# Kernel tuning notes

Hardware: AMD Instinct MI355X
Metric: run time of the kernel (lower is better)

## Reference

```python
import jax, jax.numpy as jnp
import numpy as np

HEADS = 8
DIM_HEAD = 64
QUERY_DIM = 1024
CONTEXT_DIM = 768
INNER = HEADS * DIM_HEAD  # 512


def setup_inputs() -> dict:
    key = jax.random.key(0)
    ks = jax.random.split(key, 8)
    b, n, j = 4, 2048, 2048
    x = jax.random.normal(ks[0], (b, n, QUERY_DIM), dtype=jnp.float32)
    context = jax.random.normal(ks[1], (b, j, CONTEXT_DIM), dtype=jnp.float32)
    mask = jax.random.randint(ks[2], (b, j), 0, 2).astype(jnp.bool_)
    # weights stored as (in, out) so forward is x @ W (torch Linear stores transpose)
    W_q = jax.random.normal(ks[3], (QUERY_DIM, INNER), dtype=jnp.float32) / np.sqrt(QUERY_DIM)
    W_k = jax.random.normal(ks[4], (CONTEXT_DIM, INNER), dtype=jnp.float32) / np.sqrt(CONTEXT_DIM)
    W_v = jax.random.normal(ks[5], (CONTEXT_DIM, INNER), dtype=jnp.float32) / np.sqrt(CONTEXT_DIM)
    W_o = jax.random.normal(ks[6], (INNER, QUERY_DIM), dtype=jnp.float32) / np.sqrt(INNER)
    b_o = jax.random.normal(ks[7], (QUERY_DIM,), dtype=jnp.float32) * 0.01
    return {"x": x, "context": context, "mask": mask,
            "W_q": W_q, "W_k": W_k, "W_v": W_v, "W_o": W_o, "b_o": b_o}


def reference(x, context, mask, W_q, W_k, W_v, W_o, b_o):
    b, n, _ = x.shape
    j = context.shape[1]
    scale = DIM_HEAD ** -0.5
    # projections -> [b, n, h, d]
    q = (x @ W_q).reshape(b, n, HEADS, DIM_HEAD)
    k = (context @ W_k).reshape(b, j, HEADS, DIM_HEAD)
    v = (context @ W_v).reshape(b, j, HEADS, DIM_HEAD)
    # similarity [b, h, n, j]
    sim = jnp.einsum('bihd,bjhd->bhij', q, k) * scale
    max_neg = -jnp.finfo(sim.dtype).max
    sim = jnp.where(mask[:, None, None, :], sim, max_neg)
    attn = jax.nn.softmax(sim, axis=-1)
    out = jnp.einsum('bhij,bjhd->bihd', attn, v).reshape(b, n, INNER)
    return out @ W_o + b_o  # dropout is identity (p=0 / eval)
```

## Files before the change

### kernel.cpp

```cpp
#include <hip/hip_runtime.h>
#include <hip/hip_bf16.h>

typedef __attribute__((ext_vector_type(4)))  float  f32x4;
typedef __attribute__((ext_vector_type(16))) float  f32x16;
typedef __attribute__((ext_vector_type(8)))  short  bf16x8;
typedef __attribute__((ext_vector_type(4)))  int    int32x4;
typedef __attribute__((ext_vector_type(2)))  unsigned int uint32x2;

#define DEVINL static __device__ __forceinline__
#define GAS __attribute__((address_space(1)))
#define LAS __attribute__((address_space(3)))

DEVINL ushort f2bf(float f) {
  unsigned u = __builtin_bit_cast(unsigned, f);
  unsigned r = u + 0x7fffu + ((u >> 16) & 1u);
  return (ushort)(r >> 16);
}

DEVINL unsigned cvtpk(float lo, float hi) {
  unsigned r;
  asm("v_cvt_pk_bf16_f32 %0, %1, %2" : "=v"(r) : "v"(lo), "v"(hi));
  return r;
}

DEVINL void plswap(unsigned &a, unsigned &b) {
  asm("v_permlane32_swap_b32 %0, %1" : "+v"(a), "+v"(b));
}

DEVINL float bf2f(short s) {
  return __builtin_bit_cast(float, ((unsigned)(ushort)s) << 16);
}

DEVINL f32x4 mfma16(bf16x8 a, bf16x8 b, f32x4 c) {
  return __builtin_amdgcn_mfma_f32_16x16x32_bf16(a, b, c, 0, 0, 0);
}
DEVINL f32x16 mfma32(bf16x8 a, bf16x8 b, f32x16 c) {
  return __builtin_amdgcn_mfma_f32_32x32x16_bf16(a, b, c, 0, 0, 0);
}

__global__ __launch_bounds__(256)
void cvt_k(const float* __restrict__ x, const float* __restrict__ ctx,
           ushort* __restrict__ xb, ushort* __restrict__ cb,
           const int* __restrict__ msk, float* __restrict__ mb)
{
  const int NX = 8388608, NC = 6291456;
  int tid = blockIdx.x * 256 + threadIdx.x;
  if (tid < 8192) mb[tid] = msk[tid] ? 0.f : -1e30f;
  for (int i = tid; i < (NX + NC) / 8; i += 2048 * 256) {
    int e = i * 8;
    const float* s; ushort* d;
    if (e < NX) { s = x + e; d = xb + e; }
    else        { s = ctx + (e - NX); d = cb + (e - NX); }
    f32x4 v0 = *(const f32x4*)s;
    f32x4 v1 = *(const f32x4*)(s + 4);
    union { unsigned u[4]; int32x4 v; } pk;
    pk.u[0] = cvtpk(v0[0], v0[1]);
    pk.u[1] = cvtpk(v0[2], v0[3]);
    pk.u[2] = cvtpk(v1[0], v1[1]);
    pk.u[3] = cvtpk(v1[2], v1[3]);
    *(int32x4*)d = pk.v;
  }
}

__global__ __launch_bounds__(256)
void wtcvt_k(const float* __restrict__ Wq, const float* __restrict__ Wk,
             const float* __restrict__ Wv, const float* __restrict__ Wo,
             ushort* __restrict__ WqT, ushort* __restrict__ WkT,
             ushort* __restrict__ WvT, ushort* __restrict__ WoT)
{
  __shared__ ushort Ts[64][72];
  int id = blockIdx.x;
  const float* src; ushort* dst; int Kd, Nd, lid;
  if (id < 128)      { src = Wq; dst = WqT; Kd = 1024; Nd = 512;  lid = id; }
  else if (id < 224) { src = Wk; dst = WkT; Kd = 768;  Nd = 512;  lid = id - 128; }
  else if (id < 320) { src = Wv; dst = WvT; Kd = 768;  Nd = 512;  lid = id - 224; }
  else               { src = Wo; dst = WoT; Kd = 512;  Nd = 1024; lid = id - 320; }
  const int sh = (Nd == 512) ? 3 : 4;
  const int kb = lid >> sh, nb = lid & ((1 << sh) - 1);
  const int k0 = kb * 64, n0 = nb * 64;
  const int t = threadIdx.x;
  const int r = t >> 2, c0 = (t & 3) * 16;

  const float* sp = src + (size_t)(k0 + r) * Nd + n0 + c0;
  f32x4 v0 = *(const f32x4*)(sp);
  f32x4 v1 = *(const f32x4*)(sp + 4);
  f32x4 v2 = *(const f32x4*)(sp + 8);
  f32x4 v3 = *(const f32x4*)(sp + 12);
  #pragma unroll
  for (int e = 0; e < 4; e++) {
    Ts[c0 + e][r]      = f2bf(v0[e]);
    Ts[c0 + 4 + e][r]  = f2bf(v1[e]);
    Ts[c0 + 8 + e][r]  = f2bf(v2[e]);
    Ts[c0 + 12 + e][r] = f2bf(v3[e]);
  }
  __syncthreads();
  const int n = t >> 2, kc = (t & 3) * 16;
  bf16x8 o0 = *(const bf16x8*)&Ts[n][kc];
  bf16x8 o1 = *(const bf16x8*)&Ts[n][kc + 8];
  ushort* dp = dst + (size_t)(n0 + n) * Kd + k0 + kc;
  *(bf16x8*)dp       = o0;
  *(bf16x8*)(dp + 8) = o1;
}

template<int PHASE>
__global__ __launch_bounds__(256)
void mm_k(const ushort* __restrict__ xb, const ushort* __restrict__ cb,
          const ushort* __restrict__ WqT, const ushort* __restrict__ WkT,
          const ushort* __restrict__ WvT,
          ushort* __restrict__ Qb, ushort* __restrict__ Kb, ushort* __restrict__ VT,
          const ushort* __restrict__ AO, const ushort* __restrict__ WoT,
          float* __restrict__ out, const float* __restrict__ bias)
{
  __shared__ ushort As[2][128 * 32];
  __shared__ ushort Bs[2][128 * 32];

  const ushort* A; const ushort* BT; ushort* Cw = nullptr;
  int Kd, mode, m0, n0;
  if (PHASE == 0) {
    int id = blockIdx.x;
    id = (id & 7) * 96 + (id >> 3);
    const int which = id >> 8, local = id & 255;
    m0 = (local >> 2) * 128; n0 = (local & 3) * 128;
    if (which == 0)      { A = xb; BT = WqT; Cw = Qb; Kd = 1024; mode = 1; }
    else if (which == 1) { A = cb; BT = WkT; Cw = Kb; Kd = 768;  mode = 1; }
    else                 { A = cb; BT = WvT; Cw = VT; Kd = 768;  mode = 2; }
  } else {
    int id = blockIdx.x;
    id = (id & 7) * 64 + (id >> 3);
    m0 = (id >> 3) * 128; n0 = (id & 7) * 128;
    A = AO; BT = WoT; Kd = 512; mode = 0;
  }

  const int t = threadIdx.x, lane = t & 63, w = t >> 6;
  const int wr = w >> 1, wc = w & 1;
  const int g = lane >> 4, ql = lane & 15;

  const int srowo = 16 * w + (lane >> 2);
  const int sgg = (lane & 3) ^ ((lane >> 3) & 3);

  f32x4 acc[4][4];
  #pragma unroll
  for (int i = 0; i < 4; i++)
    #pragma unroll
    for (int j = 0; j < 4; j++) acc[i][j] = (f32x4){0.f, 0.f, 0.f, 0.f};

  auto stage = [&](int buf, int k0) {
    #pragma unroll
    for (int i = 0; i < 2; i++) {
      const int row = i * 64 + srowo;
      const ushort* asrc = A + (size_t)(m0 + row) * Kd + k0 + sgg * 8;
      __builtin_amdgcn_global_load_lds((const GAS void*)asrc,
          (LAS void*)&As[buf][(i * 64 + 16 * w) * 32], 16, 0, 0);
      const ushort* bsrc = BT + (size_t)(n0 + row) * Kd + k0 + sgg * 8;
      __builtin_amdgcn_global_load_lds((const GAS void*)bsrc,
          (LAS void*)&Bs[buf][(i * 64 + 16 * w) * 32], 16, 0, 0);
    }
  };

  const int NK = Kd >> 5;
  stage(0, 0);
  __syncthreads();

  const int sel = (ql >> 1) & 3;
  const int koff = (g ^ sel) * 8;

  for (int tt = 0; tt < NK; tt++) {
    const int cur = tt & 1;
    if (tt + 1 < NK) stage(cur ^ 1, (tt + 1) * 32);

    bf16x8 af[4], bfr[4];
    #pragma unroll
    for (int i = 0; i < 4; i++) {
      af[i]  = *(const bf16x8*)&As[cur][(wr * 64 + i * 16 + ql) * 32 + koff];
      bfr[i] = *(const bf16x8*)&Bs[cur][(wc * 64 + i * 16 + ql) * 32 + koff];
    }
    #pragma unroll
    for (int i = 0; i < 4; i++)
      #pragma unroll
      for (int j = 0; j < 4; j++)
        acc[i][j] = mfma16(af[i], bfr[j], acc[i][j]);
    __syncthreads();
  }

  #pragma unroll
  for (int i = 0; i < 4; i++) {
    #pragma unroll
    for (int j = 0; j < 4; j++) {
      int col = n0 + wc * 64 + j * 16 + ql;
      #pragma unroll
      for (int r = 0; r < 4; r++) {
        int mrow = m0 + wr * 64 + i * 16 + g * 4 + r;
        float v = acc[i][j][r];
        if (PHASE == 1) {
          out[(size_t)mrow * 1024 + col] = v + bias[col];
        } else {
          int b = mrow >> 11, nn = mrow & 2047;
          int hh = col >> 6, dd = col & 63;
          size_t base = (size_t)(b * 8 + hh) * 131072;
          if (mode == 1) Cw[base + (size_t)nn * 64 + dd]   = f2bf(v);
          else           Cw[base + (size_t)dd * 2048 + nn] = f2bf(v);
        }
      }
    }
  }
}

__global__ __launch_bounds__(256)
void attn_k(const ushort* __restrict__ Qb, const ushort* __restrict__ Kb,
            const ushort* __restrict__ VT, const float* __restrict__ mb,
            ushort* __restrict__ Opart, float2* __restrict__ Ml)
{
  constexpr int CHUNK = 512, NT = CHUNK / 64;
  __shared__ ushort Ks[2][64 * 64];
  __shared__ ushort Vs[2][64 * 64];

  const int bh = blockIdx.x, b = bh >> 3;
  const int sp = blockIdx.z;
  const int jb = sp * CHUNK;
  const int t = threadIdx.x, lane = t & 63, w = t >> 6;
  const int l31 = lane & 31, hi = lane >> 5;
  const int q0 = blockIdx.y * 128 + w * 32;

  const ushort* Qh = Qb + (size_t)bh * 131072;
  const ushort* Kh = Kb + (size_t)bh * 131072;
  const ushort* Vh = VT + (size_t)bh * 131072;
  const float* mp = mb + b * 2048 + 4 * hi;

  const int srow = lane >> 3;
  const int soff = ((lane & 7) * 16) ^ ((srow & 7) << 4);

  auto stage = [&](int buf, int j0) {
    const char* kg = (const char*)Kh + ((size_t)(j0 + 16 * w + srow)) * 128 + soff;
    __builtin_amdgcn_global_load_lds((const GAS void*)kg,
        (LAS void*)&Ks[buf][16 * w * 64], 16, 0, 0);
    __builtin_amdgcn_global_load_lds((const GAS void*)(kg + 1024),
        (LAS void*)&Ks[buf][(16 * w + 8) * 64], 16, 0, 0);
    const char* vg = (const char*)Vh + ((size_t)(16 * w + srow)) * 4096 + (size_t)j0 * 2 + soff;
    __builtin_amdgcn_global_load_lds((const GAS void*)vg,
        (LAS void*)&Vs[buf][16 * w * 64], 16, 0, 0);
    __builtin_amdgcn_global_load_lds((const GAS void*)(vg + 8 * 4096),
        (LAS void*)&Vs[buf][(16 * w + 8) * 64], 16, 0, 0);
  };

  bf16x8 qf[4];
  #pragma unroll
  for (int kk = 0; kk < 4; kk++)
    qf[kk] = *(const bf16x8*)(Qh + (size_t)(q0 + l31) * 64 + kk * 16 + 8 * hi);

  f32x16 o0 = {}, o1 = {};
  float m = -1e30f, lsum = 0.f;
  const float sc = 0.18033688011112042f;

  stage(0, jb);
  __syncthreads();

  for (int tt = 0; tt < NT; ++tt) {
    const int cur = tt & 1;
    if (tt + 1 < NT) stage(cur ^ 1, jb + (tt + 1) * 64);

    #pragma unroll
    for (int js = 0; js < 2; ++js) {
      const int jloc = js * 32;
      const int j0 = jb + tt * 64 + jloc;

      f32x4 mb0 = *(const f32x4*)(mp + j0);
      f32x4 mb1 = *(const f32x4*)(mp + j0 + 8);
      f32x4 mb2 = *(const f32x4*)(mp + j0 + 16);
      f32x4 mb3 = *(const f32x4*)(mp + j0 + 24);

      const int krow = jloc + l31;
      const unsigned rsw = (unsigned)((l31 & 7) << 4);
      const char* kbase = (const char*)&Ks[cur][0] + krow * 128;
      bf16x8 kf0 = *(const bf16x8*)(kbase + ((0  + hi * 16) ^ rsw));
      bf16x8 kf1 = *(const bf16x8*)(kbase + ((32 + hi * 16) ^ rsw));
      bf16x8 kf2 = *(const bf16x8*)(kbase + ((64 + hi * 16) ^ rsw));
      bf16x8 kf3 = *(const bf16x8*)(kbase + ((96 + hi * 16) ^ rsw));

      __builtin_amdgcn_s_setprio(1);
      f32x16 z = {};
      f32x16 s = mfma32(kf0, qf[0], z);
      s = mfma32(kf1, qf[1], s);
      s = mfma32(kf2, qf[2], s);
      s = mfma32(kf3, qf[3], s);
      __builtin_amdgcn_s_setprio(0);

      const char* vb0 = (const char*)&Vs[cur][0] + l31 * 128;
      const char* vb1 = vb0 + 32 * 128;
      const unsigned vc0 = (unsigned)((jloc * 2 + hi * 16) ^ rsw);
      const unsigned vc1 = (unsigned)((jloc * 2 + 32 + hi * 16) ^ rsw);
      bf16x8 vf00 = *(const bf16x8*)(vb0 + vc0);
      bf16x8 vf01 = *(const bf16x8*)(vb0 + vc1);
      bf16x8 vf10 = *(const bf16x8*)(vb1 + vc0);
      bf16x8 vf11 = *(const bf16x8*)(vb1 + vc1);

      float pv[16];
      #pragma unroll
      for (int e = 0; e < 4; e++) {
        pv[e]      = fmaf(s[e],      sc, mb0[e]);
        pv[4 + e]  = fmaf(s[4 + e],  sc, mb1[e]);
        pv[8 + e]  = fmaf(s[8 + e],  sc, mb2[e]);
        pv[12 + e] = fmaf(s[12 + e], sc, mb3[e]);
      }

      float t0 = fmaxf(fmaxf(pv[0],  pv[1]),  pv[2]);
      float t1 = fmaxf(fmaxf(pv[3],  pv[4]),  pv[5]);
      float t2 = fmaxf(fmaxf(pv[6],  pv[7]),  pv[8]);
      float t3 = fmaxf(fmaxf(pv[9],  pv[10]), pv[11]);
      float t4 = fmaxf(fmaxf(pv[12], pv[13]), pv[14]);
      float pm = fmaxf(fmaxf(fmaxf(t0, t1), t2), fmaxf(fmaxf(t3, t4), pv[15]));
      pm = fmaxf(pm, __shfl_xor(pm, 32));

      if (!__all(pm <= m + 8.f)) {
        float mn = fmaxf(m, pm);
        float al = exp2f(m - mn);
        lsum *= al;
        #pragma unroll
        for (int r = 0; r < 16; r++) { o0[r] *= al; o1[r] *= al; }
        m = mn;
      }

      #pragma unroll
      for (int r = 0; r < 16; r++) pv[r] = exp2f(pv[r] - m);
      float a0 = (pv[0] + pv[1]) + (pv[2] + pv[3]);
      float a1 = (pv[4] + pv[5]) + (pv[6] + pv[7]);
      float a2 = (pv[8] + pv[9]) + (pv[10] + pv[11]);
      float a3 = (pv[12] + pv[13]) + (pv[14] + pv[15]);
      float rs = (a0 + a1) + (a2 + a3);
      rs += __shfl_xor(rs, 32);
      lsum += rs;

      unsigned pk01 = cvtpk(pv[0],  pv[1]),  pk23 = cvtpk(pv[2],  pv[3]);
      unsigned pk45 = cvtpk(pv[4],  pv[5]),  pk67 = cvtpk(pv[6],  pv[7]);
      unsigned pk89 = cvtpk(pv[8],  pv[9]),  pkAB = cvtpk(pv[10], pv[11]);
      unsigned pkCD = cvtpk(pv[12], pv[13]), pkEF = cvtpk(pv[14], pv[15]);
      plswap(pk01, pk45);
      plswap(pk23, pk67);
      plswap(pk89, pkCD);
      plswap(pkAB, pkEF);
      union { unsigned u[4]; bf16x8 v; } pf0, pf1;
      pf0.u[0] = pk01; pf0.u[1] = pk23; pf0.u[2] = pk45; pf0.u[3] = pk67;
      pf1.u[0] = pk89; pf1.u[1] = pkAB; pf1.u[2] = pkCD; pf1.u[3] = pkEF;

      __builtin_amdgcn_s_setprio(1);
      o0 = mfma32(vf00, pf0.v, o0);
      o0 = mfma32(vf01, pf1.v, o0);
      o1 = mfma32(vf10, pf0.v, o1);
      o1 = mfma32(vf11, pf1.v, o1);
      __builtin_amdgcn_s_setprio(0);
    }
    __syncthreads();
  }

  float inv = lsum > 0.f ? 1.0f / lsum : 0.f;
  const int q = q0 + l31;
  ushort* op = Opart + (size_t)sp * 4194304 + ((size_t)(bh * 2048 + q)) * 64;
  #pragma unroll
  for (int grp = 0; grp < 4; grp++) {
    int d0 = grp * 8 + 4 * hi;
    uint32x2 w0, w1;
    w0[0] = cvtpk(o0[4 * grp] * inv, o0[4 * grp + 1] * inv);
    w0[1] = cvtpk(o0[4 * grp + 2] * inv, o0[4 * grp + 3] * inv);
    w1[0] = cvtpk(o1[4 * grp] * inv, o1[4 * grp + 1] * inv);
    w1[1] = cvtpk(o1[4 * grp + 2] * inv, o1[4 * grp + 3] * inv);
    *(uint32x2*)(op + d0)      = w0;
    *(uint32x2*)(op + 32 + d0) = w1;
  }
  if (hi == 0) {
    float2 v; v.x = m; v.y = lsum;
    Ml[sp * 65536 + bh * 2048 + q] = v;
  }
}

__global__ __launch_bounds__(256)
void reduce_k(const ushort* __restrict__ Opart, const float2* __restrict__ Ml,
              ushort* __restrict__ AO)
{
  const int idx = blockIdx.x * 256 + threadIdx.x;
  const int d8 = idx & 7, q = (idx >> 3) & 2047, bh = idx >> 14;
  const int b = bh >> 3, h = bh & 7;

  float2 ml[4];
  float M = -1e30f;
  #pragma unroll
  for (int s = 0; s < 4; s++) {
    ml[s] = Ml[s * 65536 + bh * 2048 + q];
    M = fmaxf(M, ml[s].x);
  }
  float wgt[4], L = 0.f;
  #pragma unroll
  for (int s = 0; s < 4; s++) {
    wgt[s] = ml[s].y * exp2f(ml[s].x - M);
    L += wgt[s];
  }
  float invL = 1.f / L;

  float acc[8] = {0.f,0.f,0.f,0.f,0.f,0.f,0.f,0.f};
  #pragma unroll
  for (int s = 0; s < 4; s++) {
    bf16x8 v = *(const bf16x8*)(Opart + (size_t)s * 4194304 +
                                ((size_t)(bh * 2048 + q)) * 64 + d8 * 8);
    float ws = wgt[s] * invL;
    #pragma unroll
    for (int e = 0; e < 8; e++) acc[e] += ws * bf2f(v[e]);
  }

  union { unsigned u[4]; int32x4 v; } pk;
  pk.u[0] = cvtpk(acc[0], acc[1]);
  pk.u[1] = cvtpk(acc[2], acc[3]);
  pk.u[2] = cvtpk(acc[4], acc[5]);
  pk.u[3] = cvtpk(acc[6], acc[7]);
  *(int32x4*)(AO + ((size_t)(b * 2048 + q)) * 512 + h * 64 + d8 * 8) = pk.v;
}

extern "C" void kernel_launch(void* const* d_in, const int* in_sizes, int n_in,
                              void* d_out, int out_size, void* d_ws, size_t ws_size,
                              hipStream_t stream)
{
  const float* x   = (const float*)d_in[0];
  const float* ctx = (const float*)d_in[1];
  const int*   mk  = (const int*)d_in[2];
  const float* Wq  = (const float*)d_in[3];
  const float* Wk  = (const float*)d_in[4];
  const float* Wv  = (const float*)d_in[5];
  const float* Wo  = (const float*)d_in[6];
  const float* bo  = (const float*)d_in[7];
  float* out = (float*)d_out;

  ushort* Qb  = (ushort*)d_ws;
  ushort* Kb  = Qb + 4194304;
  ushort* VT  = Kb + 4194304;
  ushort* WoT = VT + 4194304;
  float*  mb  = (float*)(WoT + 524288);
  ushort* R2  = WoT + 524288 + 16384;
  ushort* xb  = R2;
  ushort* cb  = xb + 8388608;
  ushort* WqT = cb + 6291456;
  ushort* WkT = WqT + 524288;
  ushort* WvT = WkT + 393216;
  ushort* Opart = R2;
  float2* Ml    = (float2*)(R2 + 16777216);
  ushort* AO    = Qb;

  cvt_k<<<2048, 256, 0, stream>>>(x, ctx, xb, cb, mk, mb);
  wtcvt_k<<<448, 256, 0, stream>>>(Wq, Wk, Wv, Wo, WqT, WkT, WvT, WoT);
  mm_k<0><<<768, 256, 0, stream>>>(xb, cb, WqT, WkT, WvT, Qb, Kb, VT,
                                   nullptr, nullptr, nullptr, nullptr);
  attn_k<<<dim3(32, 16, 4), 256, 0, stream>>>(Qb, Kb, VT, mb, Opart, Ml);
  reduce_k<<<2048, 256, 0, stream>>>(Opart, Ml, AO);
  mm_k<1><<<512, 256, 0, stream>>>(nullptr, nullptr, nullptr, nullptr, nullptr,
                                   nullptr, nullptr, nullptr, AO, WoT, out, bo);
}
```

Before: 162.3 us.

## Process two 32-row query tiles per wave to reuse K/V fragments

```diff
diff --git a/kernel.cpp b/kernel.cpp
--- a/kernel.cpp
+++ b/kernel.cpp
@@ -219,7 +219,7 @@
   const int jb = sp * CHUNK;
   const int t = threadIdx.x, lane = t & 63, w = t >> 6;
   const int l31 = lane & 31, hi = lane >> 5;
-  const int q0 = blockIdx.y * 128 + w * 32;
+  const int q0 = blockIdx.y * 256 + w * 64;
 
   const ushort* Qh = Qb + (size_t)bh * 131072;
   const ushort* Kh = Kb + (size_t)bh * 131072;
@@ -242,13 +242,15 @@
         (LAS void*)&Vs[buf][(16 * w + 8) * 64], 16, 0, 0);
   };
 
-  bf16x8 qf[4];
-  #pragma unroll
-  for (int kk = 0; kk < 4; kk++)
-    qf[kk] = *(const bf16x8*)(Qh + (size_t)(q0 + l31) * 64 + kk * 16 + 8 * hi);
-
-  f32x16 o0 = {}, o1 = {};
-  float m = -1e30f, lsum = 0.f;
+  bf16x8 qfa[4], qfb[4];
+  #pragma unroll
+  for (int kk = 0; kk < 4; kk++) {
+    qfa[kk] = *(const bf16x8*)(Qh + (size_t)(q0 + l31) * 64 + kk * 16 + 8 * hi);
+    qfb[kk] = *(const bf16x8*)(Qh + (size_t)(q0 + 32 + l31) * 64 + kk * 16 + 8 * hi);
+  }
+
+  f32x16 oa0 = {}, oa1 = {}, ob0 = {}, ob1 = {};
+  float m_a = -1e30f, l_a = 0.f, m_b = -1e30f, l_b = 0.f;
   const float sc = 0.18033688011112042f;
 
   stage(0, jb);
@@ -263,10 +265,10 @@
       const int jloc = js * 32;
       const int j0 = jb + tt * 64 + jloc;
 
-      f32x4 mb0 = *(const f32x4*)(mp + j0);
-      f32x4 mb1 = *(const f32x4*)(mp + j0 + 8);
-      f32x4 mb2 = *(const f32x4*)(mp + j0 + 16);
-      f32x4 mb3 = *(const f32x4*)(mp + j0 + 24);
+      f32x4 bia0 = *(const f32x4*)(mp + j0);
+      f32x4 bia1 = *(const f32x4*)(mp + j0 + 8);
+      f32x4 bia2 = *(const f32x4*)(mp + j0 + 16);
+      f32x4 bia3 = *(const f32x4*)(mp + j0 + 24);
 
       const int krow = jloc + l31;
       const unsigned rsw = (unsigned)((l31 & 7) << 4);
@@ -278,10 +280,14 @@
 
       __builtin_amdgcn_s_setprio(1);
       f32x16 z = {};
-      f32x16 s = mfma32(kf0, qf[0], z);
-      s = mfma32(kf1, qf[1], s);
-      s = mfma32(kf2, qf[2], s);
-      s = mfma32(kf3, qf[3], s);
+      f32x16 sa = mfma32(kf0, qfa[0], z);
+      f32x16 sb = mfma32(kf0, qfb[0], z);
+      sa = mfma32(kf1, qfa[1], sa);
+      sb = mfma32(kf1, qfb[1], sb);
+      sa = mfma32(kf2, qfa[2], sa);
+      sb = mfma32(kf2, qfb[2], sb);
+      sa = mfma32(kf3, qfa[3], sa);
+      sb = mfma32(kf3, qfb[3], sb);
       __builtin_amdgcn_s_setprio(0);
 
       const char* vb0 = (const char*)&Vs[cur][0] + l31 * 128;
@@ -293,81 +299,134 @@
       bf16x8 vf10 = *(const bf16x8*)(vb1 + vc0);
       bf16x8 vf11 = *(const bf16x8*)(vb1 + vc1);
 
-      float pv[16];
+      float pva[16], pvb[16];
       #pragma unroll
       for (int e = 0; e < 4; e++) {
-        pv[e]      = fmaf(s[e],      sc, mb0[e]);
-        pv[4 + e]  = fmaf(s[4 + e],  sc, mb1[e]);
-        pv[8 + e]  = fmaf(s[8 + e],  sc, mb2[e]);
-        pv[12 + e] = fmaf(s[12 + e], sc, mb3[e]);
+        pva[e]      = fmaf(sa[e],      sc, bia0[e]);
+        pva[4 + e]  = fmaf(sa[4 + e],  sc, bia1[e]);
+        pva[8 + e]  = fmaf(sa[8 + e],  sc, bia2[e]);
+        pva[12 + e] = fmaf(sa[12 + e], sc, bia3[e]);
+        pvb[e]      = fmaf(sb[e],      sc, bia0[e]);
+        pvb[4 + e]  = fmaf(sb[4 + e],  sc, bia1[e]);
+        pvb[8 + e]  = fmaf(sb[8 + e],  sc, bia2[e]);
+        pvb[12 + e] = fmaf(sb[12 + e], sc, bia3[e]);
       }
 
-      float t0 = fmaxf(fmaxf(pv[0],  pv[1]),  pv[2]);
-      float t1 = fmaxf(fmaxf(pv[3],  pv[4]),  pv[5]);
-      float t2 = fmaxf(fmaxf(pv[6],  pv[7]),  pv[8]);
-      float t3 = fmaxf(fmaxf(pv[9],  pv[10]), pv[11]);
-      float t4 = fmaxf(fmaxf(pv[12], pv[13]), pv[14]);
-      float pm = fmaxf(fmaxf(fmaxf(t0, t1), t2), fmaxf(fmaxf(t3, t4), pv[15]));
-      pm = fmaxf(pm, __shfl_xor(pm, 32));
-
-      if (!__all(pm <= m + 8.f)) {
-        float mn = fmaxf(m, pm);
-        float al = exp2f(m - mn);
-        lsum *= al;
+      float ta0 = fmaxf(fmaxf(pva[0],  pva[1]),  pva[2]);
+      float ta1 = fmaxf(fmaxf(pva[3],  pva[4]),  pva[5]);
+      float ta2 = fmaxf(fmaxf(pva[6],  pva[7]),  pva[8]);
+      float ta3 = fmaxf(fmaxf(pva[9],  pva[10]), pva[11]);
+      float ta4 = fmaxf(fmaxf(pva[12], pva[13]), pva[14]);
+      float pma = fmaxf(fmaxf(fmaxf(ta0, ta1), ta2), fmaxf(fmaxf(ta3, ta4), pva[15]));
+      pma = fmaxf(pma, __shfl_xor(pma, 32));
+
+      float tb0 = fmaxf(fmaxf(pvb[0],  pvb[1]),  pvb[2]);
+      float tb1 = fmaxf(fmaxf(pvb[3],  pvb[4]),  pvb[5]);
+      float tb2 = fmaxf(fmaxf(pvb[6],  pvb[7]),  pvb[8]);
+      float tb3 = fmaxf(fmaxf(pvb[9],  pvb[10]), pvb[11]);
+      float tb4 = fmaxf(fmaxf(pvb[12], pvb[13]), pvb[14]);
+      float pmb = fmaxf(fmaxf(fmaxf(tb0, tb1), tb2), fmaxf(fmaxf(tb3, tb4), pvb[15]));
+      pmb = fmaxf(pmb, __shfl_xor(pmb, 32));
+
+      if (!__all(pma <= m_a + 8.f)) {
+        float mn = fmaxf(m_a, pma);
+        float al = exp2f(m_a - mn);
+        l_a *= al;
         #pragma unroll
-        for (int r = 0; r < 16; r++) { o0[r] *= al; o1[r] *= al; }
-        m = mn;
+        for (int r = 0; r < 16; r++) { oa0[r] *= al; oa1[r] *= al; }
+        m_a = mn;
       }
+      if (!__all(pmb <= m_b + 8.f)) {
+        float mn = fmaxf(m_b, pmb);
+        float al = exp2f(m_b - mn);
+        l_b *= al;
+        #pragma unroll
+        for (int r = 0; r < 16; r++) { ob0[r] *= al; ob1[r] *= al; }
+        m_b = mn;
+      }
 
       #pragma unroll
-      for (int r = 0; r < 16; r++) pv[r] = exp2f(pv[r] - m);
-      float a0 = (pv[0] + pv[1]) + (pv[2] + pv[3]);
-      float a1 = (pv[4] + pv[5]) + (pv[6] + pv[7]);
-      float a2 = (pv[8] + pv[9]) + (pv[10] + pv[11]);
-      float a3 = (pv[12] + pv[13]) + (pv[14] + pv[15]);
-      float rs = (a0 + a1) + (a2 + a3);
-      rs += __shfl_xor(rs, 32);
-      lsum += rs;
-
-      unsigned pk01 = cvtpk(pv[0],  pv[1]),  pk23 = cvtpk(pv[2],  pv[3]);
-      unsigned pk45 = cvtpk(pv[4],  pv[5]),  pk67 = cvtpk(pv[6],  pv[7]);
-      unsigned pk89 = cvtpk(pv[8],  pv[9]),  pkAB = cvtpk(pv[10], pv[11]);
-      unsigned pkCD = cvtpk(pv[12], pv[13]), pkEF = cvtpk(pv[14], pv[15]);
-      plswap(pk01, pk45);
-      plswap(pk23, pk67);
-      plswap(pk89, pkCD);
-      plswap(pkAB, pkEF);
-      union { unsigned u[4]; bf16x8 v; } pf0, pf1;
-      pf0.u[0] = pk01; pf0.u[1] = pk23; pf0.u[2] = pk45; pf0.u[3] = pk67;
-      pf1.u[0] = pk89; pf1.u[1] = pkAB; pf1.u[2] = pkCD; pf1.u[3] = pkEF;
+      for (int r = 0; r < 16; r++) { pva[r] = exp2f(pva[r] - m_a); pvb[r] = exp2f(pvb[r] - m_b); }
+      float aa0 = (pva[0] + pva[1]) + (pva[2] + pva[3]);
+      float aa1 = (pva[4] + pva[5]) + (pva[6] + pva[7]);
+      float aa2 = (pva[8] + pva[9]) + (pva[10] + pva[11]);
+      float aa3 = (pva[12] + pva[13]) + (pva[14] + pva[15]);
+      float rsa = (aa0 + aa1) + (aa2 + aa3);
+      rsa += __shfl_xor(rsa, 32);
+      l_a += rsa;
+      float ab0 = (pvb[0] + pvb[1]) + (pvb[2] + pvb[3]);
+      float ab1 = (pvb[4] + pvb[5]) + (pvb[6] + pvb[7]);
+      float ab2 = (pvb[8] + pvb[9]) + (pvb[10] + pvb[11]);
+      float ab3 = (pvb[12] + pvb[13]) + (pvb[14] + pvb[15]);
+      float rsb = (ab0 + ab1) + (ab2 + ab3);
+      rsb += __shfl_xor(rsb, 32);
+      l_b += rsb;
+
+      unsigned a01 = cvtpk(pva[0],  pva[1]),  a23 = cvtpk(pva[2],  pva[3]);
+      unsigned a45 = cvtpk(pva[4],  pva[5]),  a67 = cvtpk(pva[6],  pva[7]);
+      unsigned a89 = cvtpk(pva[8],  pva[9]),  aAB = cvtpk(pva[10], pva[11]);
+      unsigned aCD = cvtpk(pva[12], pva[13]), aEF = cvtpk(pva[14], pva[15]);
+      plswap(a01, a45);
+      plswap(a23, a67);
+      plswap(a89, aCD);
+      plswap(aAB, aEF);
+      union { unsigned u[4]; bf16x8 v; } pf0a, pf1a, pf0b, pf1b;
+      pf0a.u[0] = a01; pf0a.u[1] = a23; pf0a.u[2] = a45; pf0a.u[3] = a67;
+      pf1a.u[0] = a89; pf1a.u[1] = aAB; pf1a.u[2] = aCD; pf1a.u[3] = aEF;
+
+      unsigned b01 = cvtpk(pvb[0],  pvb[1]),  b23 = cvtpk(pvb[2],  pvb[3]);
+      unsigned b45 = cvtpk(pvb[4],  pvb[5]),  b67 = cvtpk(pvb[6],  pvb[7]);
+      unsigned b89 = cvtpk(pvb[8],  pvb[9]),  bAB = cvtpk(pvb[10], pvb[11]);
+      unsigned bCD = cvtpk(pvb[12], pvb[13]), bEF = cvtpk(pvb[14], pvb[15]);
+      plswap(b01, b45);
+      plswap(b23, b67);
+      plswap(b89, bCD);
+      plswap(bAB, bEF);
+      pf0b.u[0] = b01; pf0b.u[1] = b23; pf0b.u[2] = b45; pf0b.u[3] = b67;
+      pf1b.u[0] = b89; pf1b.u[1] = bAB; pf1b.u[2] = bCD; pf1b.u[3] = bEF;
 
       __builtin_amdgcn_s_setprio(1);
-      o0 = mfma32(vf00, pf0.v, o0);
-      o0 = mfma32(vf01, pf1.v, o0);
-      o1 = mfma32(vf10, pf0.v, o1);
-      o1 = mfma32(vf11, pf1.v, o1);
+      oa0 = mfma32(vf00, pf0a.v, oa0);
+      ob0 = mfma32(vf00, pf0b.v, ob0);
+      oa0 = mfma32(vf01, pf1a.v, oa0);
+      ob0 = mfma32(vf01, pf1b.v, ob0);
+      oa1 = mfma32(vf10, pf0a.v, oa1);
+      ob1 = mfma32(vf10, pf0b.v, ob1);
+      oa1 = mfma32(vf11, pf1a.v, oa1);
+      ob1 = mfma32(vf11, pf1b.v, ob1);
       __builtin_amdgcn_s_setprio(0);
     }
     __syncthreads();
   }
 
-  float inv = lsum > 0.f ? 1.0f / lsum : 0.f;
-  const int q = q0 + l31;
-  ushort* op = Opart + (size_t)sp * 4194304 + ((size_t)(bh * 2048 + q)) * 64;
+  float inva = l_a > 0.f ? 1.0f / l_a : 0.f;
+  float invb = l_b > 0.f ? 1.0f / l_b : 0.f;
+  const int qa = q0 + l31, qb2 = q0 + 32 + l31;
+  ushort* opa = Opart + (size_t)sp * 4194304 + ((size_t)(bh * 2048 + qa)) * 64;
+  ushort* opb = Opart + (size_t)sp * 4194304 + ((size_t)(bh * 2048 + qb2)) * 64;
   #pragma unroll
   for (int grp = 0; grp < 4; grp++) {
     int d0 = grp * 8 + 4 * hi;
     uint32x2 w0, w1;
-    w0[0] = cvtpk(o0[4 * grp] * inv, o0[4 * grp + 1] * inv);
-    w0[1] = cvtpk(o0[4 * grp + 2] * inv, o0[4 * grp + 3] * inv);
-    w1[0] = cvtpk(o1[4 * grp] * inv, o1[4 * grp + 1] * inv);
-    w1[1] = cvtpk(o1[4 * grp + 2] * inv, o1[4 * grp + 3] * inv);
-    *(uint32x2*)(op + d0)      = w0;
-    *(uint32x2*)(op + 32 + d0) = w1;
+    w0[0] = cvtpk(oa0[4 * grp] * inva, oa0[4 * grp + 1] * inva);
+    w0[1] = cvtpk(oa0[4 * grp + 2] * inva, oa0[4 * grp + 3] * inva);
+    w1[0] = cvtpk(oa1[4 * grp] * inva, oa1[4 * grp + 1] * inva);
+    w1[1] = cvtpk(oa1[4 * grp + 2] * inva, oa1[4 * grp + 3] * inva);
+    *(uint32x2*)(opa + d0)      = w0;
+    *(uint32x2*)(opa + 32 + d0) = w1;
+    uint32x2 x0, x1;
+    x0[0] = cvtpk(ob0[4 * grp] * invb, ob0[4 * grp + 1] * invb);
+    x0[1] = cvtpk(ob0[4 * grp + 2] * invb, ob0[4 * grp + 3] * invb);
+    x1[0] = cvtpk(ob1[4 * grp] * invb, ob1[4 * grp + 1] * invb);
+    x1[1] = cvtpk(ob1[4 * grp + 2] * invb, ob1[4 * grp + 3] * invb);
+    *(uint32x2*)(opb + d0)      = x0;
+    *(uint32x2*)(opb + 32 + d0) = x1;
   }
   if (hi == 0) {
-    float2 v; v.x = m; v.y = lsum;
-    Ml[sp * 65536 + bh * 2048 + q] = v;
+    float2 va; va.x = m_a; va.y = l_a;
+    Ml[sp * 65536 + bh * 2048 + qa] = va;
+    float2 vb; vb.x = m_b; vb.y = l_b;
+    Ml[sp * 65536 + bh * 2048 + qb2] = vb;
   }
 }
 
@@ -445,7 +504,7 @@
   wtcvt_k<<<448, 256, 0, stream>>>(Wq, Wk, Wv, Wo, WqT, WkT, WvT, WoT);
   mm_k<0><<<768, 256, 0, stream>>>(xb, cb, WqT, WkT, WvT, Qb, Kb, VT,
                                    nullptr, nullptr, nullptr, nullptr);
-  attn_k<<<dim3(32, 16, 4), 256, 0, stream>>>(Qb, Kb, VT, mb, Opart, Ml);
+  attn_k<<<dim3(32, 8, 4), 256, 0, stream>>>(Qb, Kb, VT, mb, Opart, Ml);
   reduce_k<<<2048, 256, 0, stream>>>(Opart, Ml, AO);
   mm_k<1><<<512, 256, 0, stream>>>(nullptr, nullptr, nullptr, nullptr, nullptr,
                                    nullptr, nullptr, nullptr, AO, WoT, out, bo);
```

New measurement: 204.1 us. 1.26x slower.
